# Performance work log

Measured on AMD Instinct MI355X. Metric: run time of the kernel, lower is better.

Reference implementation:

```python
import jax, jax.numpy as jnp
import numpy as np

N, E, IN_FT, OUT_FT = 20000, 4096, 128, 128


def setup_inputs() -> dict:
    key = jax.random.key(0)
    kx, kh, kw = jax.random.split(key, 3)
    X = jax.random.normal(kx, (N, IN_FT), dtype=jnp.float32)
    H = jax.random.randint(kh, (N, E), 0, 2, dtype=jnp.int32)
    weight = jax.random.normal(kw, (IN_FT, OUT_FT), dtype=jnp.float32) * (1.0 / np.sqrt(IN_FT))
    bias = jnp.zeros((OUT_FT,), dtype=jnp.float32)
    return {"X": X, "H": H, "weight": weight, "bias": bias}


def reference(X, H, weight, bias):
    # Dv^{-1/2} H De^{-1} H^T Dv^{-1/2} X W + b, with diag matrices fused as
    # row/column scalings (same math as the torch.diag @ chain, no NxN temporaries).
    Hf = H.astype(jnp.float32)
    v_deg = jnp.sum(Hf, axis=1)            # [N]
    e_deg = jnp.sum(Hf, axis=0)            # [E]
    v_deg = jnp.where(v_deg > 0, v_deg, 1.0)
    e_deg = jnp.where(e_deg > 0, e_deg, 1.0)
    dv_inv_sqrt = 1.0 / jnp.sqrt(v_deg)    # diag(Dv^-1/2)
    de_inv = 1.0 / e_deg                   # diag(De^-1)
    Y = dv_inv_sqrt[:, None] * X
    T = Hf.T @ Y                           # H^T (...)        [E, in]
    T = de_inv[:, None] * T                # De^-1 (...)
    Z = Hf @ T                             # H (...)          [N, in]
    Z = dv_inv_sqrt[:, None] * Z           # Dv^-1/2 (...)
    out = Z @ weight + bias                # [N, out]
    return out
```

## Files before the change

kernel.cpp:

```cpp
#include <hip/hip_runtime.h>

#define NV 20000
#define NE 4096
#define FT 128
#define NW_E 128
#define NKC2 157
#define K_TOT 20096

typedef __attribute__((ext_vector_type(8))) short short8v;
typedef __attribute__((ext_vector_type(4))) float float4v;

__device__ __forceinline__ unsigned short f2bf(float f) {
    unsigned u = __float_as_uint(f);
    u += 0x7FFFu + ((u >> 16) & 1u);
    return (unsigned short)(u >> 16);
}
__device__ __forceinline__ int lds_off(int r, int c) {
    return r * 256 + ((c ^ (r & 15)) << 4);
}
__device__ __forceinline__ uint4 lut_entry(int t) {
    uint4 e;
    e.x = ((t & 1) ? 0x3F80u : 0u) | ((t & 2) ? 0x3F800000u : 0u);
    e.y = ((t & 4) ? 0x3F80u : 0u) | ((t & 8) ? 0x3F800000u : 0u);
    e.z = ((t & 16) ? 0x3F80u : 0u) | ((t & 32) ? 0x3F800000u : 0u);
    e.w = ((t & 64) ? 0x3F80u : 0u) | ((t & 128) ? 0x3F800000u : 0u);
    return e;
}
__device__ __forceinline__ void cp16(void* l, const void* g) {
    __builtin_amdgcn_global_load_lds((__attribute__((address_space(1))) void*)g,
                                     (__attribute__((address_space(3))) void*)l, 16, 0, 0);
}
__device__ __forceinline__ unsigned bt32(unsigned x, int lane) {
    unsigned y;
    y = __shfl_xor(x, 16, 64);
    x = (lane & 16) ? ((x & 0xFFFF0000u) | ((y >> 16) & 0x0000FFFFu))
                    : ((x & 0x0000FFFFu) | ((y << 16) & 0xFFFF0000u));
    y = __shfl_xor(x, 8, 64);
    x = (lane & 8)  ? ((x & 0xFF00FF00u) | ((y >> 8) & 0x00FF00FFu))
                    : ((x & 0x00FF00FFu) | ((y << 8) & 0xFF00FF00u));
    y = __shfl_xor(x, 4, 64);
    x = (lane & 4)  ? ((x & 0xF0F0F0F0u) | ((y >> 4) & 0x0F0F0F0Fu))
                    : ((x & 0x0F0F0F0Fu) | ((y << 4) & 0xF0F0F0F0u));
    y = __shfl_xor(x, 2, 64);
    x = (lane & 2)  ? ((x & 0xCCCCCCCCu) | ((y >> 2) & 0x33333333u))
                    : ((x & 0x33333333u) | ((y << 2) & 0xCCCCCCCCu));
    y = __shfl_xor(x, 1, 64);
    x = (lane & 1)  ? ((x & 0xAAAAAAAAu) | ((y >> 1) & 0x55555555u))
                    : ((x & 0x55555555u) | ((y << 1) & 0xAAAAAAAAu));
    return x;
}

__global__ __launch_bounds__(256) void k_pack(const int* __restrict__ H,
                                              unsigned* __restrict__ packed,
                                              float* __restrict__ dv,
                                              int* __restrict__ de_cnt) {
    __shared__ int cl[4];
    int t = threadIdx.x, wave = t >> 6, lane = t & 63;
    if (blockIdx.x < 16) de_cnt[blockIdx.x * 256 + t] = 0;
    int row = blockIdx.x * 2 + (wave >> 1);
    int half = wave & 1;
    const uint4* base = reinterpret_cast<const uint4*>(H) + (size_t)row * 1024 + half * 512 + lane * 8;
    unsigned m = 0;
#pragma unroll
    for (int i = 0; i < 8; ++i) {
        uint4 v = base[i];
        m |= (v.x ? 1u : 0u) << (i * 4 + 0);
        m |= (v.y ? 1u : 0u) << (i * 4 + 1);
        m |= (v.z ? 1u : 0u) << (i * 4 + 2);
        m |= (v.w ? 1u : 0u) << (i * 4 + 3);
    }
    packed[(size_t)row * NW_E + half * 64 + lane] = m;
    int c = __popc(m);
    for (int o = 32; o > 0; o >>= 1) c += __shfl_down(c, o, 64);
    if (lane == 0) cl[wave] = c;
    __syncthreads();
    if (t < 2) {
        int d = cl[t * 2] + cl[t * 2 + 1];
        dv[blockIdx.x * 2 + t] = d > 0 ? 1.0f / sqrtf((float)d) : 1.0f;
    }
}

__global__ __launch_bounds__(256) void k_mid(const float* __restrict__ X,
                                             const float* __restrict__ dv,
                                             unsigned short* __restrict__ At) {
    int t = threadIdx.x;
    int f = t & 127;
    int item = blockIdx.x * 2 + (t >> 7);
    int nbase = item * 8;
    unsigned short h[8];
#pragma unroll
    for (int i = 0; i < 8; ++i) {
        int n = nbase + i;
        float v = (n < NV) ? X[(size_t)n * FT + f] * dv[n] : 0.0f;
        h[i] = f2bf(v);
    }
    uint4 u;
    u.x = (unsigned)h[0] | ((unsigned)h[1] << 16);
    u.y = (unsigned)h[2] | ((unsigned)h[3] << 16);
    u.z = (unsigned)h[4] | ((unsigned)h[5] << 16);
    u.w = (unsigned)h[6] | ((unsigned)h[7] << 16);
    int kc2 = nbase >> 7;
    int c = (nbase >> 3) & 15;
    *reinterpret_cast<uint4*>(At + (size_t)kc2 * 16384 + f * 128 + ((c ^ (f & 15)) << 3)) = u;
}

__global__ __launch_bounds__(256, 2) void k_mm1(const unsigned short* __restrict__ At,
                                                const unsigned* __restrict__ packed,
                                                float* __restrict__ P,
                                                int* __restrict__ de_cnt, int chunkK) {
    __shared__ __align__(16) unsigned char sA[32768];
    __shared__ __align__(16) unsigned char sB[32768];
    __shared__ __align__(16) uint4 slut[256];
    int t = threadIdx.x;
    slut[t] = lut_entry(t);

    int et = blockIdx.x & 31, kp = blockIdx.x >> 5;
    int e0 = et * 128;
    int kbeg = kp * chunkK;
    int kend = kbeg + chunkK; if (kend > K_TOT) kend = K_TOT;
    int iters = (kend - kbeg) >> 7; if (iters < 0) iters = 0;

    float4v acc[4][4];
#pragma unroll
    for (int i = 0; i < 4; ++i)
#pragma unroll
        for (int j = 0; j < 4; ++j)
#pragma unroll
            for (int r = 0; r < 4; ++r) acc[i][j][r] = 0.0f;

    int wave = t >> 6, lane = t & 63;
    int wm0 = (wave & 1) * 64, wc0 = (wave >> 1) * 64;
    int r0 = lane & 15, q = lane >> 4;

    int grp = t >> 5, l32 = t & 31;
    int ns = grp & 3;
    int wbase = (grp >> 2) * 2;
    int ecol = et * 4 + wbase;
    int de_c0 = 0, de_c1 = 0;

    auto ldB = [&](int it) {
        uint2 v; v.x = 0u; v.y = 0u;
        int n = kbeg + it * 128 + ns * 32 + l32;
        if (n < NV) v = *reinterpret_cast<const uint2*>(packed + (size_t)n * NW_E + ecol);
        return v;
    };
    uint2 bw; bw.x = 0u; bw.y = 0u;
    if (iters > 0) bw = ldB(0);
    __syncthreads();

    const char* gA = reinterpret_cast<const char*>(At) + (size_t)(kbeg >> 7) * 32768 + wave * 8192 + lane * 16;
    char* lA = reinterpret_cast<char*>(sA) + wave * 8192;

    int rB0 = wbase * 32 + l32;
    int rB1 = rB0 + 32;

    for (int it = 0; it < iters; ++it) {
        const char* g = gA + (size_t)it * 32768;
#pragma unroll
        for (int j = 0; j < 8; ++j) cp16(lA + j * 1024, g + j * 1024);
        uint2 nxt; nxt.x = 0u; nxt.y = 0u;
        if (it + 1 < iters) nxt = ldB(it + 1);
        {
            unsigned x0 = bt32(bw.x, lane);
            unsigned x1 = bt32(bw.y, lane);
            de_c0 += __popc(x0);
            de_c1 += __popc(x1);
#pragma unroll
            for (int c = 0; c < 4; ++c)
                *reinterpret_cast<uint4*>(sB + lds_off(rB0, ns * 4 + c)) = slut[(x0 >> (c * 8)) & 0xFF];
#pragma unroll
            for (int c = 0; c < 4; ++c)
                *reinterpret_cast<uint4*>(sB + lds_off(rB1, ns * 4 + c)) = slut[(x1 >> (c * 8)) & 0xFF];
            bw = nxt;
        }
        __syncthreads();
#pragma unroll
        for (int ks = 0; ks < 4; ++ks) {
            short8v a[4], bb[4];
#pragma unroll
            for (int mi = 0; mi < 4; ++mi)
                a[mi] = *reinterpret_cast<const short8v*>(sA + lds_off(wm0 + mi * 16 + r0, ks * 4 + q));
#pragma unroll
            for (int ci = 0; ci < 4; ++ci)
                bb[ci] = *reinterpret_cast<const short8v*>(sB + lds_off(wc0 + ci * 16 + r0, ks * 4 + q));
#pragma unroll
            for (int mi = 0; mi < 4; ++mi)
#pragma unroll
                for (int ci = 0; ci < 4; ++ci)
                    acc[mi][ci] = __builtin_amdgcn_mfma_f32_16x16x32_bf16(a[mi], bb[ci], acc[mi][ci], 0, 0, 0);
        }
        __syncthreads();
    }
    atomicAdd(de_cnt + e0 + rB0, de_c0);
    atomicAdd(de_cnt + e0 + rB1, de_c1);
    float* Pp = P + (size_t)kp * (4096 * 128);
#pragma unroll
    for (int mi = 0; mi < 4; ++mi)
#pragma unroll
        for (int ci = 0; ci < 4; ++ci) {
            int f = wm0 + mi * 16 + q * 4;
            int e = e0 + wc0 + ci * 16 + r0;
            *reinterpret_cast<float4v*>(Pp + (size_t)e * 128 + f) = acc[mi][ci];
        }
}

__global__ __launch_bounds__(256) void k_redut(const float* __restrict__ P,
                                               const float* __restrict__ W,
                                               const int* __restrict__ de_cnt,
                                               unsigned short* __restrict__ Ut,
                                               float* __restrict__ out,
                                               const float* __restrict__ bias, int S) {
    __shared__ float sT[8][132];
    int t = threadIdx.x;
    {
        const float4* b4 = reinterpret_cast<const float4*>(bias);
        float4* o4 = reinterpret_cast<float4*>(out);
        for (int i = blockIdx.x * 256 + t; i < NV * 32; i += 512 * 256)
            o4[i] = b4[i & 31];
    }
    int e0 = blockIdx.x * 8;
    {
        int el = t >> 5, fq = (t & 31) * 4;
        const float* base = P + (size_t)(e0 + el) * 128 + fq;
        float4 s = {0.f, 0.f, 0.f, 0.f};
        for (int p = 0; p < S; ++p) {
            float4 v = *reinterpret_cast<const float4*>(base + (size_t)p * 524288);
            s.x += v.x; s.y += v.y; s.z += v.z; s.w += v.w;
        }
        *reinterpret_cast<float4*>(&sT[el][fq]) = s;
    }
    __syncthreads();
    int el = t & 7, gq = (t >> 3) * 4;
    int e = e0 + el;
    float a0 = 0, a1 = 0, a2 = 0, a3 = 0;
    for (int f = 0; f < 128; ++f) {
        float tv = sT[el][f];
        float4 wv = *reinterpret_cast<const float4*>(W + f * 128 + gq);
        a0 += tv * wv.x; a1 += tv * wv.y; a2 += tv * wv.z; a3 += tv * wv.w;
    }
    int cnt = de_cnt[e];
    float d = cnt > 0 ? 1.0f / (float)cnt : 1.0f;
    float av[4] = {a0, a1, a2, a3};
    int slabB = e >> 7, chi = (e >> 3) & 15, pos = e & 7;
#pragma unroll
    for (int k = 0; k < 4; ++k) {
        int g = gq + k, qg = g >> 5, gr = g & 31;
        Ut[(size_t)(qg * 32 + slabB) * 4096 + gr * 128 + ((chi ^ (gr & 15)) << 3) + pos] = f2bf(av[k] * d);
    }
}

__global__ __launch_bounds__(256, 2) void k_mm2(const unsigned* __restrict__ packed,
                                                const unsigned short* __restrict__ Ut,
                                                const float* __restrict__ dv,
                                                float* __restrict__ out) {
    __shared__ __align__(16) unsigned char sA[32768];
    __shared__ __align__(16) unsigned char sB[32768];
    __shared__ __align__(16) uint4 slut[256];
    int t = threadIdx.x;
    slut[t] = lut_entry(t);

    int mt = blockIdx.x >> 2, es = blockIdx.x & 3;
    int n0 = mt * 128;

    float4v acc[4][4];
#pragma unroll
    for (int i = 0; i < 4; ++i)
#pragma unroll
        for (int j = 0; j < 4; ++j)
#pragma unroll
            for (int r = 0; r < 4; ++r) acc[i][j][r] = 0.0f;

    int wave = t >> 6, lane = t & 63;
    int wm0 = (wave & 1) * 64, wg0 = (wave >> 1) * 64;
    int r0 = lane & 15, q = lane >> 4;

    int rA = t & 127, half = t >> 7, cb = half << 3;
    const uint4* arow4 = reinterpret_cast<const uint4*>(packed + (size_t)(n0 + rA) * NW_E) + es * 8;
    uint4 aw = arow4[0];
    __syncthreads();

    const char* gB = reinterpret_cast<const char*>(Ut) + ((size_t)wave * 32 + es * 8) * 8192 + lane * 16;
    char* lB = reinterpret_cast<char*>(sB) + wave * 8192;

    for (int it = 0; it < 8; ++it) {
        uint4 nxt = arow4[it + 1];
        {
            const char* g = gB + (size_t)it * 8192;
#pragma unroll
            for (int j = 0; j < 8; ++j) cp16(lB + j * 1024, g + j * 1024);
        }
        {
            unsigned wd0 = half ? aw.z : aw.x;
            unsigned wd1 = half ? aw.w : aw.y;
#pragma unroll
            for (int c = 0; c < 4; ++c)
                *reinterpret_cast<uint4*>(sA + lds_off(rA, cb + c)) = slut[(wd0 >> (c * 8)) & 0xFF];
#pragma unroll
            for (int c = 0; c < 4; ++c)
                *reinterpret_cast<uint4*>(sA + lds_off(rA, cb + 4 + c)) = slut[(wd1 >> (c * 8)) & 0xFF];
            aw = nxt;
        }
        __syncthreads();
#pragma unroll
        for (int ks = 0; ks < 4; ++ks) {
            short8v a[4], bb[4];
#pragma unroll
            for (int mi = 0; mi < 4; ++mi)
                a[mi] = *reinterpret_cast<const short8v*>(sA + lds_off(wm0 + mi * 16 + r0, ks * 4 + q));
#pragma unroll
            for (int ci = 0; ci < 4; ++ci)
                bb[ci] = *reinterpret_cast<const short8v*>(sB + lds_off(wg0 + ci * 16 + r0, ks * 4 + q));
#pragma unroll
            for (int mi = 0; mi < 4; ++mi)
#pragma unroll
                for (int ci = 0; ci < 4; ++ci)
                    acc[mi][ci] = __builtin_amdgcn_mfma_f32_16x16x32_bf16(a[mi], bb[ci], acc[mi][ci], 0, 0, 0);
        }
        __syncthreads();
    }
#pragma unroll
    for (int mi = 0; mi < 4; ++mi)
#pragma unroll
        for (int ci = 0; ci < 4; ++ci) {
            int g = wg0 + ci * 16 + r0;
#pragma unroll
            for (int r = 0; r < 4; ++r) {
                int n = n0 + wm0 + mi * 16 + q * 4 + r;
                if (n < NV) atomicAdd(out + (size_t)n * 128 + g, dv[n] * acc[mi][ci][r]);
            }
        }
}

extern "C" void kernel_launch(void* const* d_in, const int* in_sizes, int n_in,
                              void* d_out, int out_size, void* d_ws, size_t ws_size,
                              hipStream_t stream) {
    const float* X    = (const float*)d_in[0];
    const int*   H    = (const int*)d_in[1];
    const float* W    = (const float*)d_in[2];
    const float* bias = (const float*)d_in[3];
    float* out = (float*)d_out;

    char* ws = (char*)d_ws;
    size_t off = 0;
    auto alloc = [&](size_t sz) { char* p = ws + off; off += (sz + 255) & ~(size_t)255; return p; };
    unsigned*       packed  = (unsigned*)alloc((size_t)NV * NW_E * 4);
    unsigned short* At      = (unsigned short*)alloc((size_t)NKC2 * 16384 * 2);
    unsigned short* Ut      = (unsigned short*)alloc((size_t)FT * NE * 2);
    float*          dv      = (float*)alloc((size_t)NV * 4);
    int*            de_cnt  = (int*)alloc((size_t)NE * 4);
    size_t fixed = off;

    long long avail = (long long)ws_size - (long long)fixed;
    int S = (int)(avail / (128LL * 4096 * 4));
    if (S > 16) S = 16;
    if (S < 1) S = 1;
    float* P1 = (float*)(ws + fixed);
    int chunkK = ((NKC2 + S - 1) / S) * 128;

    k_pack  <<<NV / 2, 256, 0, stream>>>(H, packed, dv, de_cnt);
    k_mid   <<<1256, 256, 0, stream>>>(X, dv, At);
    k_mm1   <<<32 * S, 256, 0, stream>>>(At, packed, P1, de_cnt, chunkK);
    k_redut <<<512, 256, 0, stream>>>(P1, W, de_cnt, Ut, out, bias, S);
    k_mm2   <<<628, 256, 0, stream>>>(packed, Ut, dv, out);
}
```

Before: 570.3 us.

## Replace mm2 atomic output with split partials and a final reduce kernel

k_mm2 used to scatter its four edge-split partial products into the output with per-element float atomics scaled by dv. It now writes plain stores into a padded partial buffer, and a new k_final kernel sums the four partials, applies the dv scaling and adds the bias. The bias pre-fill moves out of k_redut. Separately, the shared-memory byte-to-bf16 lookup table is replaced by computing the expansion inline in registers, which removes a barrier. This trades atomic contention for extra buffer traffic of roughly 41 MB and one more launch.

New measurement: 547.3 us (median of 2 runs). 1.04x faster.

```diff
diff --git a/kernel.cpp b/kernel.cpp
--- a/kernel.cpp
+++ b/kernel.cpp
@@ -6,6 +6,7 @@
 #define NW_E 128
 #define NKC2 157
 #define K_TOT 20096
+#define NPAD 20096
 
 typedef __attribute__((ext_vector_type(8))) short short8v;
 typedef __attribute__((ext_vector_type(4))) float float4v;
@@ -18,12 +19,12 @@
 __device__ __forceinline__ int lds_off(int r, int c) {
     return r * 256 + ((c ^ (r & 15)) << 4);
 }
-__device__ __forceinline__ uint4 lut_entry(int t) {
+__device__ __forceinline__ uint4 expand8v(unsigned b) {
     uint4 e;
-    e.x = ((t & 1) ? 0x3F80u : 0u) | ((t & 2) ? 0x3F800000u : 0u);
-    e.y = ((t & 4) ? 0x3F80u : 0u) | ((t & 8) ? 0x3F800000u : 0u);
-    e.z = ((t & 16) ? 0x3F80u : 0u) | ((t & 32) ? 0x3F800000u : 0u);
-    e.w = ((t & 64) ? 0x3F80u : 0u) | ((t & 128) ? 0x3F800000u : 0u);
+    e.x = ((b & 1u)   ? 0x3F80u : 0u) | ((b & 2u)   ? 0x3F800000u : 0u);
+    e.y = ((b & 4u)   ? 0x3F80u : 0u) | ((b & 8u)   ? 0x3F800000u : 0u);
+    e.z = ((b & 16u)  ? 0x3F80u : 0u) | ((b & 32u)  ? 0x3F800000u : 0u);
+    e.w = ((b & 64u)  ? 0x3F80u : 0u) | ((b & 128u) ? 0x3F800000u : 0u);
     return e;
 }
 __device__ __forceinline__ void cp16(void* l, const void* g) {
@@ -110,9 +111,7 @@
                                                 int* __restrict__ de_cnt, int chunkK) {
     __shared__ __align__(16) unsigned char sA[32768];
     __shared__ __align__(16) unsigned char sB[32768];
-    __shared__ __align__(16) uint4 slut[256];
     int t = threadIdx.x;
-    slut[t] = lut_entry(t);
 
     int et = blockIdx.x & 31, kp = blockIdx.x >> 5;
     int e0 = et * 128;
@@ -146,7 +145,6 @@
     };
     uint2 bw; bw.x = 0u; bw.y = 0u;
     if (iters > 0) bw = ldB(0);
-    __syncthreads();
 
     const char* gA = reinterpret_cast<const char*>(At) + (size_t)(kbeg >> 7) * 32768 + wave * 8192 + lane * 16;
     char* lA = reinterpret_cast<char*>(sA) + wave * 8192;
@@ -167,10 +165,10 @@
             de_c1 += __popc(x1);
 #pragma unroll
             for (int c = 0; c < 4; ++c)
-                *reinterpret_cast<uint4*>(sB + lds_off(rB0, ns * 4 + c)) = slut[(x0 >> (c * 8)) & 0xFF];
+                *reinterpret_cast<uint4*>(sB + lds_off(rB0, ns * 4 + c)) = expand8v(x0 >> (c * 8));
 #pragma unroll
             for (int c = 0; c < 4; ++c)
-                *reinterpret_cast<uint4*>(sB + lds_off(rB1, ns * 4 + c)) = slut[(x1 >> (c * 8)) & 0xFF];
+                *reinterpret_cast<uint4*>(sB + lds_off(rB1, ns * 4 + c)) = expand8v(x1 >> (c * 8));
             bw = nxt;
         }
         __syncthreads();
@@ -207,17 +205,9 @@
 __global__ __launch_bounds__(256) void k_redut(const float* __restrict__ P,
                                                const float* __restrict__ W,
                                                const int* __restrict__ de_cnt,
-                                               unsigned short* __restrict__ Ut,
-                                               float* __restrict__ out,
-                                               const float* __restrict__ bias, int S) {
+                                               unsigned short* __restrict__ Ut, int S) {
     __shared__ float sT[8][132];
     int t = threadIdx.x;
-    {
-        const float4* b4 = reinterpret_cast<const float4*>(bias);
-        float4* o4 = reinterpret_cast<float4*>(out);
-        for (int i = blockIdx.x * 256 + t; i < NV * 32; i += 512 * 256)
-            o4[i] = b4[i & 31];
-    }
     int e0 = blockIdx.x * 8;
     {
         int el = t >> 5, fq = (t & 31) * 4;
@@ -251,13 +241,10 @@
 
 __global__ __launch_bounds__(256, 2) void k_mm2(const unsigned* __restrict__ packed,
                                                 const unsigned short* __restrict__ Ut,
-                                                const float* __restrict__ dv,
-                                                float* __restrict__ out) {
+                                                float* __restrict__ P2) {
     __shared__ __align__(16) unsigned char sA[32768];
     __shared__ __align__(16) unsigned char sB[32768];
-    __shared__ __align__(16) uint4 slut[256];
     int t = threadIdx.x;
-    slut[t] = lut_entry(t);
 
     int mt = blockIdx.x >> 2, es = blockIdx.x & 3;
     int n0 = mt * 128;
@@ -277,7 +264,6 @@
     int rA = t & 127, half = t >> 7, cb = half << 3;
     const uint4* arow4 = reinterpret_cast<const uint4*>(packed + (size_t)(n0 + rA) * NW_E) + es * 8;
     uint4 aw = arow4[0];
-    __syncthreads();
 
     const char* gB = reinterpret_cast<const char*>(Ut) + ((size_t)wave * 32 + es * 8) * 8192 + lane * 16;
     char* lB = reinterpret_cast<char*>(sB) + wave * 8192;
@@ -294,10 +280,10 @@
             unsigned wd1 = half ? aw.w : aw.y;
 #pragma unroll
             for (int c = 0; c < 4; ++c)
-                *reinterpret_cast<uint4*>(sA + lds_off(rA, cb + c)) = slut[(wd0 >> (c * 8)) & 0xFF];
+                *reinterpret_cast<uint4*>(sA + lds_off(rA, cb + c)) = expand8v(wd0 >> (c * 8));
 #pragma unroll
             for (int c = 0; c < 4; ++c)
-                *reinterpret_cast<uint4*>(sA + lds_off(rA, cb + 4 + c)) = slut[(wd1 >> (c * 8)) & 0xFF];
+                *reinterpret_cast<uint4*>(sA + lds_off(rA, cb + 4 + c)) = expand8v(wd1 >> (c * 8));
             aw = nxt;
         }
         __syncthreads();
@@ -318,6 +304,7 @@
         }
         __syncthreads();
     }
+    float* p = P2 + (size_t)es * NPAD * 128;
 #pragma unroll
     for (int mi = 0; mi < 4; ++mi)
 #pragma unroll
@@ -326,9 +313,24 @@
 #pragma unroll
             for (int r = 0; r < 4; ++r) {
                 int n = n0 + wm0 + mi * 16 + q * 4 + r;
-                if (n < NV) atomicAdd(out + (size_t)n * 128 + g, dv[n] * acc[mi][ci][r]);
+                p[(size_t)n * 128 + g] = acc[mi][ci][r];
             }
         }
+}
+
+__global__ __launch_bounds__(256) void k_final(const float* __restrict__ P2,
+                                               const float* __restrict__ dv,
+                                               const float* __restrict__ bias,
+                                               float* __restrict__ out) {
+    int i = blockIdx.x * 256 + threadIdx.x;
+    if (i >= NV * 32) return;
+    int n = i >> 5, g4 = i & 31;
+    const float4v* p = reinterpret_cast<const float4v*>(P2) + (size_t)n * 32 + g4;
+    const size_t esS = (size_t)NPAD * 32;
+    float4v s = p[0] + p[esS] + p[2 * esS] + p[3 * esS];
+    float d = dv[n];
+    float4v b = reinterpret_cast<const float4v*>(bias)[g4];
+    reinterpret_cast<float4v*>(out)[(size_t)n * 32 + g4] = s * d + b;
 }
 
 extern "C" void kernel_launch(void* const* d_in, const int* in_sizes, int n_in,
@@ -348,6 +350,7 @@
     unsigned short* Ut      = (unsigned short*)alloc((size_t)FT * NE * 2);
     float*          dv      = (float*)alloc((size_t)NV * 4);
     int*            de_cnt  = (int*)alloc((size_t)NE * 4);
+    float*          P2      = (float*)alloc((size_t)4 * NPAD * 128 * 4);
     size_t fixed = off;
 
     long long avail = (long long)ws_size - (long long)fixed;
@@ -360,6 +363,7 @@
     k_pack  <<<NV / 2, 256, 0, stream>>>(H, packed, dv, de_cnt);
     k_mid   <<<1256, 256, 0, stream>>>(X, dv, At);
     k_mm1   <<<32 * S, 256, 0, stream>>>(At, packed, P1, de_cnt, chunkK);
-    k_redut <<<512, 256, 0, stream>>>(P1, W, de_cnt, Ut, out, bias, S);
-    k_mm2   <<<628, 256, 0, stream>>>(packed, Ut, dv, out);
-}
+    k_redut <<<512, 256, 0, stream>>>(P1, W, de_cnt, Ut, S);
+    k_mm2   <<<628, 256, 0, stream>>>(packed, Ut, P2);
+    k_final <<<2500, 256, 0, stream>>>(P2, dv, bias, out);
+}
```
